# Kernel tuning notes

Hardware: AMD Instinct MI355X
Metric: run time of the kernel (lower is better)

## Reference

```python
import jax, jax.numpy as jnp
import numpy as np

C = 256
INTER = C // 2


def _conv1x1(x, w, b):
    # x: [B,C,H,W], w: [O,C], b: [O] -> [B,O,H,W]
    return jnp.einsum('bchw,oc->bohw', x, w) + b[None, :, None, None]


def setup_inputs() -> dict:
    key = jax.random.key(0)
    ks = jax.random.split(key, 9)
    B, H, W = 4, 64, 64
    x = jax.random.normal(ks[0], (B, C, H, W), dtype=jnp.float32)
    s_in = 1.0 / np.sqrt(C)
    s_int = 1.0 / np.sqrt(INTER)
    return {
        'x': x,
        'w_g': jax.random.normal(ks[1], (INTER, C), jnp.float32) * s_in,
        'b_g': jax.random.normal(ks[2], (INTER,), jnp.float32) * 0.01,
        'w_theta': jax.random.normal(ks[3], (INTER, C), jnp.float32) * s_in,
        'b_theta': jax.random.normal(ks[4], (INTER,), jnp.float32) * 0.01,
        'w_phi': jax.random.normal(ks[5], (INTER, C), jnp.float32) * s_in,
        'b_phi': jax.random.normal(ks[6], (INTER,), jnp.float32) * 0.01,
        'w_W': jax.random.normal(ks[7], (C, INTER), jnp.float32) * s_int,
        'b_W': jax.random.normal(ks[8], (C,), jnp.float32) * 0.01,
    }


def reference(x, w_g, b_g, w_theta, b_theta, w_phi, b_phi, w_W, b_W):
    B, Cc, H, W = x.shape
    N = H * W
    # 1x1 conv projections -> flatten spatial to N
    g_x = _conv1x1(x, w_g, b_g).reshape(B, INTER, N).transpose(0, 2, 1)        # [B,N,I]
    theta_x = _conv1x1(x, w_theta, b_theta).reshape(B, INTER, N).transpose(0, 2, 1)  # [B,N,I]
    phi_x = _conv1x1(x, w_phi, b_phi).reshape(B, INTER, N)                     # [B,I,N]
    f = jnp.einsum('bni,bim->bnm', theta_x, phi_x)                             # [B,N,N]
    f_div_C = jax.nn.softmax(f, axis=-1)
    y = jnp.einsum('bnm,bmi->bni', f_div_C, g_x)                               # [B,N,I]
    y = y.transpose(0, 2, 1).reshape(B, INTER, H, W)
    W_y = _conv1x1(y, w_W, b_W)                                                # [B,C,H,W]
    return W_y + x
```

## Files before the change

### kernel.cpp

```cpp
#include <hip/hip_runtime.h>

typedef unsigned short ushort_t;
typedef unsigned int uint_t;
typedef _Float16 f16;
typedef __attribute__((ext_vector_type(8))) _Float16 f16x8;
typedef __attribute__((ext_vector_type(2))) _Float16 f16x2;
typedef __attribute__((ext_vector_type(4))) float f32x4;

#define B_ 4
#define C_ 256
#define I_ 128
#define N_ 4096
#define KVB 32
#define TOT_IT (N_ / KVB)
#define LOG2E 1.44269504f

#define XT_F 0ull
#define W_F  4194304ull
#define TH_F 4325376ull
#define PH_F 6422528ull
#define G3_F 8519680ull
#define YPX_F 10616832ull

__device__ __forceinline__ float exp2_hw(float x) { return __builtin_amdgcn_exp2f(x); }
__device__ __forceinline__ float log2_hw(float x) { return __builtin_amdgcn_logf(x); }

__device__ __forceinline__ f16x2 pkrtz(float a, float b) {
    auto r = __builtin_amdgcn_cvt_pkrtz(a, b);
    f16x2 o;
    __builtin_memcpy(&o, &r, sizeof(o));
    return o;
}
__device__ __forceinline__ f32x4 mfma16h(f16x8 a, f16x8 b, f32x4 c) {
    return __builtin_amdgcn_mfma_f32_16x16x32_f16(a, b, c, 0, 0, 0);
}
__device__ __forceinline__ f32x4 zero4() { f32x4 z = {0.f, 0.f, 0.f, 0.f}; return z; }
__device__ __forceinline__ void gload_lds16(const void* g, void* lds) {
    __builtin_amdgcn_global_load_lds(
        (const __attribute__((address_space(1))) void*)g,
        (__attribute__((address_space(3))) void*)lds, 16, 0, 0);
}
__device__ __forceinline__ size_t yp_off(int s) {
    return (s < 2) ? (size_t)s * 2097152ull
                   : YPX_F + (size_t)(s - 2) * 2097152ull;
}

__global__ __launch_bounds__(256) void k_transpose_x(const float* x, const float* wg,
        const float* wt, const float* wp, const float* wW, ushort_t* ws) {
    if (blockIdx.x >= 64) {
        int idx = (((blockIdx.x - 64) * 16 + blockIdx.y * 4 + blockIdx.z) * 256
                   + threadIdx.x) * 16;
        const float* src;
        int off;
        if (idx < 32768)      { src = wg; off = idx; }
        else if (idx < 65536) { src = wt; off = idx - 32768; }
        else if (idx < 98304) { src = wp; off = idx - 65536; }
        else                  { src = wW; off = idx - 98304; }
        f16 o[16];
#pragma unroll
        for (int j = 0; j < 16; ++j) o[j] = (f16)src[off + j];
        f16* wd = (f16*)(ws + W_F);
        *(uint4*)&wd[idx]     = *(uint4*)&o[0];
        *(uint4*)&wd[idx + 8] = *(uint4*)&o[8];
        return;
    }
    __shared__ float t[64][65];
    int b = blockIdx.z, c0 = blockIdx.y * 64, n0 = blockIdx.x * 64;
    int tid = threadIdx.x;
    int cl = tid & 63, ng = tid >> 6;
    const float* xp = x + ((size_t)(b * C_ + c0 + cl)) * N_ + n0 + ng * 16;
#pragma unroll
    for (int j = 0; j < 4; ++j) {
        float4 v = ((const float4*)xp)[j];
        t[cl][ng * 16 + j * 4 + 0] = v.x;
        t[cl][ng * 16 + j * 4 + 1] = v.y;
        t[cl][ng * 16 + j * 4 + 2] = v.z;
        t[cl][ng * 16 + j * 4 + 3] = v.w;
    }
    __syncthreads();
    int cg4 = tid & 3, nr = tid >> 2;
    f16 hv[16];
#pragma unroll
    for (int k = 0; k < 16; ++k) hv[k] = (f16)t[cg4 * 16 + k][nr];
    size_t dst = ((size_t)b * N_ + n0 + nr) * C_ + c0 + cg4 * 16;
    f16* xd = (f16*)(ws + XT_F);
    *(uint4*)&xd[dst]     = *(uint4*)&hv[0];
    *(uint4*)&xd[dst + 8] = *(uint4*)&hv[8];
}

__global__ __launch_bounds__(512) void k_proj_all(const float* bg, const float* bth,
                                                  const float* bph, ushort_t* ws) {
    int b = blockIdx.y, n0 = blockIdx.x * 64;
    int w = threadIdx.x >> 6, l = threadIdx.x & 63;
    int li = l & 15, lg = l >> 4;
    int wn = (w & 3) * 16;
    int ihb = (w >> 2) * 4;
    const f16* xh = (const f16*)(ws + XT_F);
    const f16* wf = (const f16*)(ws + W_F);

    f32x4 acc[3][4];
#pragma unroll
    for (int p = 0; p < 3; ++p)
#pragma unroll
        for (int t = 0; t < 4; ++t) acc[p][t] = zero4();

    size_t arow = ((size_t)b * N_ + n0 + wn + li) * C_;
#pragma unroll 2
    for (int kb = 0; kb < 8; ++kb) {
        int kc = kb * 32 + 8 * lg;
        f16x8 ah = *(const f16x8*)&xh[arow + kc];
#pragma unroll
        for (int p = 0; p < 3; ++p)
#pragma unroll
            for (int t = 0; t < 4; ++t) {
                f16x8 bw = *(const f16x8*)&wf[(size_t)p * 32768
                               + (size_t)((ihb + t) * 16 + li) * C_ + kc];
                acc[p][t] = mfma16h(ah, bw, acc[p][t]);
            }
    }
    f16* g3p = (f16*)(ws + G3_F);
    f16* thp = (f16*)(ws + TH_F);
    f16* php = (f16*)(ws + PH_F);
#pragma unroll
    for (int p = 0; p < 3; ++p) {
        const float* bias = (p == 0) ? bg : (p == 1) ? bth : bph;
#pragma unroll
        for (int t = 0; t < 4; ++t) {
            int i = (ihb + t) * 16 + li;
            float bs = bias[i];
#pragma unroll
            for (int r = 0; r < 4; ++r) {
                int n = n0 + wn + 4 * lg + r;
                float v = acc[p][t][r] + bs;
                if (p == 0) {
                    int tq = (n >> 2) & 3;
                    size_t gi = ((size_t)b * (N_ / 32) + (n >> 5)) * 4096
                              + (size_t)(tq * 128 + (i ^ (tq << 1))) * 8
                              + ((n >> 4) & 1) * 4 + (n & 3);
                    g3p[gi] = (f16)v;
                } else if (p == 1)
                    thp[((size_t)b * N_ + n) * I_ + i] = (f16)(v * LOG2E);
                else
                    php[((size_t)b * N_ + n) * I_ + i] = (f16)v;
            }
        }
    }
}

__global__ __launch_bounds__(256, 3) void k_attn(ushort_t* ws, float* lse, int splits) {
    __shared__ __align__(16) ushort_t smem[16384];
    int b = blockIdx.y, sp = blockIdx.z;
    int w = threadIdx.x >> 6, l = threadIdx.x & 63;
    int li = l & 15, lg = l >> 4;
    int q0 = blockIdx.x * 128 + w * 16;
    const f16* th = (const f16*)(ws + TH_F);
    const f16* ph = (const f16*)(ws + PH_F);
    const f16* g3 = (const f16*)(ws + G3_F);
    f16* yp = (f16*)ws + yp_off(sp);

    f16x8 qA[4], qB[4];
#pragma unroll
    for (int kb = 0; kb < 4; ++kb) {
        qA[kb] = *(const f16x8*)&th[((size_t)b * N_ + q0 + li) * I_ + kb * 32 + 8 * lg];
        qB[kb] = *(const f16x8*)&th[((size_t)b * N_ + q0 + 64 + li) * I_ + kb * 32 + 8 * lg];
    }

    f32x4 yA[8], yB[8];
#pragma unroll
    for (int dt = 0; dt < 8; ++dt) { yA[dt] = zero4(); yB[dt] = zero4(); }
    float mA = -1e30f, lA = 0.f, mB = -1e30f, lB = 0.f;

    int beg = (sp * TOT_IT) / splits;
    int end = ((sp + 1) * TOT_IT) / splits;
    int nit = end - beg;
    int srow = l >> 4;
    size_t sp0 = ((size_t)b * N_ + w * 8 + srow) * I_ + ((l & 15) ^ srow) * 8;
    size_t sp1 = ((size_t)b * N_ + w * 8 + 4 + srow) * I_ + (((l & 15) ^ srow) ^ 4) * 8;
    size_t sg0 = (size_t)b * (N_ / 32) * 4096 + w * 1024 + l * 8;

    auto stage = [&](int kv0, int bufsel) {
        int bo = bufsel * 4096;
        gload_lds16(ph + (size_t)kv0 * I_ + sp0, smem + bo + w * 1024);
        gload_lds16(ph + (size_t)kv0 * I_ + sp1, smem + bo + w * 1024 + 512);
        gload_lds16(g3 + sg0 + (size_t)kv0 * 128, smem + 8192 + bo + w * 1024);
        gload_lds16(g3 + sg0 + (size_t)kv0 * 128 + 512,
                    smem + 8192 + bo + w * 1024 + 512);
    };

    stage(beg * KVB, 0);
    __syncthreads();

    for (int it = 0; it < nit; ++it) {
        int buf = it & 1;
        if (it + 1 < nit) stage((beg + it + 1) * KVB, buf ^ 1);
        const f16* pb = (const f16*)(smem + buf * 4096);
        const f16* gbf = (const f16*)(smem + 8192 + buf * 4096);

        f32x4 fA0 = zero4(), fA1 = zero4(), fB0 = zero4(), fB1 = zero4();
        __builtin_amdgcn_s_setprio(1);
#pragma unroll
        for (int kb = 0; kb < 4; ++kb) {
            int cc = ((kb * 4 + lg) ^ (li & 7)) * 8;
            f16x8 a0 = *(const f16x8*)&pb[li * 128 + cc];
            f16x8 a1 = *(const f16x8*)&pb[(16 + li) * 128 + cc];
            fA0 = mfma16h(a0, qA[kb], fA0);
            fB0 = mfma16h(a0, qB[kb], fB0);
            fA1 = mfma16h(a1, qA[kb], fA1);
            fB1 = mfma16h(a1, qB[kb], fB1);
        }
        __builtin_amdgcn_s_setprio(0);

        float tmA = fmaxf(fmaxf(fmaxf(fA0[0], fA0[1]), fmaxf(fA0[2], fA0[3])),
                          fmaxf(fmaxf(fA1[0], fA1[1]), fmaxf(fA1[2], fA1[3])));
        tmA = fmaxf(tmA, __shfl_xor(tmA, 16));
        tmA = fmaxf(tmA, __shfl_xor(tmA, 32));
        if (__ballot(tmA > mA + 11.0f)) {
            float mn = fmaxf(mA, tmA);
            float sc = exp2_hw(mA - mn);
            lA *= sc; mA = mn;
            float s0 = __shfl(sc, 4 * lg + 0);
            float s1 = __shfl(sc, 4 * lg + 1);
            float s2 = __shfl(sc, 4 * lg + 2);
            float s3 = __shfl(sc, 4 * lg + 3);
#pragma unroll
            for (int dt = 0; dt < 8; ++dt) {
                yA[dt][0] *= s0; yA[dt][1] *= s1; yA[dt][2] *= s2; yA[dt][3] *= s3;
            }
        }
#pragma unroll
        for (int r = 0; r < 4; ++r) {
            fA0[r] = exp2_hw(fA0[r] - mA); lA += fA0[r];
            fA1[r] = exp2_hw(fA1[r] - mA); lA += fA1[r];
        }
        union PU { f16x2 h2[4]; f16x8 v; };
        PU pA;
        pA.h2[0] = pkrtz(fA0[0], fA0[1]); pA.h2[1] = pkrtz(fA0[2], fA0[3]);
        pA.h2[2] = pkrtz(fA1[0], fA1[1]); pA.h2[3] = pkrtz(fA1[2], fA1[3]);

        float tmB = fmaxf(fmaxf(fmaxf(fB0[0], fB0[1]), fmaxf(fB0[2], fB0[3])),
                          fmaxf(fmaxf(fB1[0], fB1[1]), fmaxf(fB1[2], fB1[3])));
        tmB = fmaxf(tmB, __shfl_xor(tmB, 16));
        tmB = fmaxf(tmB, __shfl_xor(tmB, 32));
        if (__ballot(tmB > mB + 11.0f)) {
            float mn = fmaxf(mB, tmB);
            float sc = exp2_hw(mB - mn);
            lB *= sc; mB = mn;
            float s0 = __shfl(sc, 4 * lg + 0);
            float s1 = __shfl(sc, 4 * lg + 1);
            float s2 = __shfl(sc, 4 * lg + 2);
            float s3 = __shfl(sc, 4 * lg + 3);
#pragma unroll
            for (int dt = 0; dt < 8; ++dt) {
                yB[dt][0] *= s0; yB[dt][1] *= s1; yB[dt][2] *= s2; yB[dt][3] *= s3;
            }
        }
#pragma unroll
        for (int r = 0; r < 4; ++r) {
            fB0[r] = exp2_hw(fB0[r] - mB); lB += fB0[r];
            fB1[r] = exp2_hw(fB1[r] - mB); lB += fB1[r];
        }
        PU pB;
        pB.h2[0] = pkrtz(fB0[0], fB0[1]); pB.h2[1] = pkrtz(fB0[2], fB0[3]);
        pB.h2[2] = pkrtz(fB1[0], fB1[1]); pB.h2[3] = pkrtz(fB1[2], fB1[3]);

        __builtin_amdgcn_s_setprio(1);
#pragma unroll
        for (int dt = 0; dt < 8; ++dt) {
            int i = dt * 16 + li;
            f16x8 gv = *(const f16x8*)&gbf[(size_t)(lg * 128 + (i ^ (lg << 1))) * 8];
            yA[dt] = mfma16h(pA.v, gv, yA[dt]);
            yB[dt] = mfma16h(pB.v, gv, yB[dt]);
        }
        __builtin_amdgcn_s_setprio(0);
        __syncthreads();
    }

    lA += __shfl_xor(lA, 16); lA += __shfl_xor(lA, 32);
    lB += __shfl_xor(lB, 16); lB += __shfl_xor(lB, 32);
    {
        float inv = 1.0f / lA;
        float i0 = __shfl(inv, 4 * lg + 0);
        float i1 = __shfl(inv, 4 * lg + 1);
        float i2 = __shfl(inv, 4 * lg + 2);
        float i3 = __shfl(inv, 4 * lg + 3);
#pragma unroll
        for (int dt = 0; dt < 8; ++dt) {
            size_t base = ((size_t)b * N_ + q0 + 4 * lg) * I_ + dt * 16 + li;
            yp[base]          = (f16)(yA[dt][0] * i0);
            yp[base + I_]     = (f16)(yA[dt][1] * i1);
            yp[base + 2 * I_] = (f16)(yA[dt][2] * i2);
            yp[base + 3 * I_] = (f16)(yA[dt][3] * i3);
        }
    }
    {
        float inv = 1.0f / lB;
        float i0 = __shfl(inv, 4 * lg + 0);
        float i1 = __shfl(inv, 4 * lg + 1);
        float i2 = __shfl(inv, 4 * lg + 2);
        float i3 = __shfl(inv, 4 * lg + 3);
#pragma unroll
        for (int dt = 0; dt < 8; ++dt) {
            size_t base = ((size_t)b * N_ + q0 + 64 + 4 * lg) * I_ + dt * 16 + li;
            yp[base]          = (f16)(yB[dt][0] * i0);
            yp[base + I_]     = (f16)(yB[dt][1] * i1);
            yp[base + 2 * I_] = (f16)(yB[dt][2] * i2);
            yp[base + 3 * I_] = (f16)(yB[dt][3] * i3);
        }
    }
    if (l < 16) {
        lse[((size_t)sp * B_ + b) * N_ + q0 + l]      = mA + log2_hw(lA);
        lse[((size_t)sp * B_ + b) * N_ + q0 + 64 + l] = mB + log2_hw(lB);
    }
}

__global__ __launch_bounds__(512) void k_out(const float* x, const float* bW,
        const ushort_t* ws, const float* lse, float* out, int splits) {
    __shared__ __align__(16) f16 ylds[64 * 136];
    int b = blockIdx.y, n0 = blockIdx.x * 64;
    int tid = threadIdx.x;
    {
        int nn = tid >> 3, ig = tid & 7;
        size_t lrow = (size_t)b * N_ + n0 + nn;
        float mx = -1e30f;
        for (int s = 0; s < splits; ++s)
            mx = fmaxf(mx, lse[(size_t)s * (B_ * N_) + lrow]);
        float sum = 0.f;
        for (int s = 0; s < splits; ++s)
            sum += exp2_hw(lse[(size_t)s * (B_ * N_) + lrow] - mx);
        float inv = 1.0f / sum;
        float acc[16];
#pragma unroll
        for (int j = 0; j < 16; ++j) acc[j] = 0.f;
        for (int s = 0; s < splits; ++s) {
            float wg = exp2_hw(lse[(size_t)s * (B_ * N_) + lrow] - mx) * inv;
            const f16* p = (const f16*)ws + yp_off(s) + lrow * I_ + ig * 16;
            f16x8 v0 = *(const f16x8*)p;
            f16x8 v1 = *(const f16x8*)(p + 8);
#pragma unroll
            for (int j = 0; j < 8; ++j) {
                acc[j]     += wg * (float)v0[j];
                acc[8 + j] += wg * (float)v1[j];
            }
        }
        f16 o[16];
#pragma unroll
        for (int j = 0; j < 16; ++j) o[j] = (f16)acc[j];
        *(uint4*)&ylds[nn * 136 + ig * 16]     = *(uint4*)&o[0];
        *(uint4*)&ylds[nn * 136 + ig * 16 + 8] = *(uint4*)&o[8];
    }
    __syncthreads();

    int w = tid >> 6, l = tid & 63;
    int li = l & 15, lg = l >> 4;
    int cw = (w >> 1) * 64, nh = (w & 1) * 32;
    const f16* wfp = (const f16*)(ws + W_F) + 98304;

    f32x4 acc2[4][2];
#pragma unroll
    for (int mm = 0; mm < 4; ++mm)
#pragma unroll
        for (int n = 0; n < 2; ++n) acc2[mm][n] = zero4();

#pragma unroll 2
    for (int kb = 0; kb < 4; ++kb) {
        int kc = kb * 32 + 8 * lg;
        f16x8 a[4], byv[2];
#pragma unroll
        for (int mm = 0; mm < 4; ++mm)
            a[mm] = *(const f16x8*)&wfp[(size_t)(cw + mm * 16 + li) * I_ + kc];
#pragma unroll
        for (int n = 0; n < 2; ++n)
            byv[n] = *(const f16x8*)&ylds[(nh + n * 16 + li) * 136 + kc];
#pragma unroll
        for (int mm = 0; mm < 4; ++mm)
#pragma unroll
            for (int n = 0; n < 2; ++n)
                acc2[mm][n] = mfma16h(a[mm], byv[n], acc2[mm][n]);
    }
#pragma unroll
    for (int mm = 0; mm < 4; ++mm)
#pragma unroll
        for (int n = 0; n < 2; ++n)
#pragma unroll
            for (int r = 0; r < 4; ++r) {
                int c = cw + mm * 16 + lg * 4 + r;
                int nn = n0 + nh + n * 16 + li;
                size_t xi = ((size_t)b * C_ + c) * N_ + nn;
                out[xi] = acc2[mm][n][r] + bW[c] + x[xi];
            }
}

extern "C" void kernel_launch(void* const* d_in, const int* in_sizes, int n_in,
                              void* d_out, int out_size, void* d_ws, size_t ws_size,
                              hipStream_t stream) {
    const float* x  = (const float*)d_in[0];
    const float* wg = (const float*)d_in[1];
    const float* bg = (const float*)d_in[2];
    const float* wt = (const float*)d_in[3];
    const float* bt = (const float*)d_in[4];
    const float* wp = (const float*)d_in[5];
    const float* bp = (const float*)d_in[6];
    const float* wW = (const float*)d_in[7];
    const float* bW = (const float*)d_in[8];
    ushort_t* ws = (ushort_t*)d_ws;
    float* out = (float*)d_out;

    int splits = (ws_size >= 46923776ull) ? 8
               : (ws_size >= 38404096ull) ? 6 : 4;
    size_t lse_off = 2ull * (YPX_F + (size_t)(splits - 2) * 2097152ull);
    float* lse = (float*)((char*)d_ws + lse_off);

    k_transpose_x<<<dim3(66, 4, 4), 256, 0, stream>>>(x, wg, wt, wp, wW, ws);
    k_proj_all<<<dim3(64, 4), 512, 0, stream>>>(bg, bt, bp, ws);
    k_attn<<<dim3(32, 4, splits), 256, 0, stream>>>(ws, lse, splits);
    k_out<<<dim3(64, 4), 512, 0, stream>>>(x, bW, ws, lse, out, splits);
}
```

Before: 110.2 us.

## Fuse x transpose into projection, unroll attention loop, raise attn occupancy

Combines the x transpose/convert with the projection GEMM, so x is transposed through LDS inside the projection kernel and the fp16 transposed copy of x is no longer written to and read back from global memory. The attention loop is manually unrolled two-way with fixed buffer offsets and precomputed LDS offsets, which removes per-iteration index arithmetic. The attention kernel's launch bound is raised to 4 blocks per SIMD. The workspace layout is compacted and a 7-split option is added. The fused kernel adds LDS use and barriers per block, and the higher occupancy target may force register spills.

```diff
diff --git a/kernel.cpp b/kernel.cpp
--- a/kernel.cpp
+++ b/kernel.cpp
@@ -15,12 +15,11 @@
 #define TOT_IT (N_ / KVB)
 #define LOG2E 1.44269504f
 
-#define XT_F 0ull
-#define W_F  4194304ull
-#define TH_F 4325376ull
-#define PH_F 6422528ull
-#define G3_F 8519680ull
-#define YPX_F 10616832ull
+#define W_F  0ull
+#define TH_F 131072ull
+#define PH_F 2228224ull
+#define G3_F 4325376ull
+#define YP_F 6422528ull
 
 __device__ __forceinline__ float exp2_hw(float x) { return __builtin_amdgcn_exp2f(x); }
 __device__ __forceinline__ float log2_hw(float x) { return __builtin_amdgcn_logf(x); }
@@ -40,82 +39,76 @@
         (const __attribute__((address_space(1))) void*)g,
         (__attribute__((address_space(3))) void*)lds, 16, 0, 0);
 }
-__device__ __forceinline__ size_t yp_off(int s) {
-    return (s < 2) ? (size_t)s * 2097152ull
-                   : YPX_F + (size_t)(s - 2) * 2097152ull;
-}
-
-__global__ __launch_bounds__(256) void k_transpose_x(const float* x, const float* wg,
-        const float* wt, const float* wp, const float* wW, ushort_t* ws) {
-    if (blockIdx.x >= 64) {
-        int idx = (((blockIdx.x - 64) * 16 + blockIdx.y * 4 + blockIdx.z) * 256
-                   + threadIdx.x) * 16;
-        const float* src;
-        int off;
-        if (idx < 32768)      { src = wg; off = idx; }
-        else if (idx < 65536) { src = wt; off = idx - 32768; }
-        else if (idx < 98304) { src = wp; off = idx - 65536; }
-        else                  { src = wW; off = idx - 98304; }
-        f16 o[16];
-#pragma unroll
-        for (int j = 0; j < 16; ++j) o[j] = (f16)src[off + j];
-        f16* wd = (f16*)(ws + W_F);
-        *(uint4*)&wd[idx]     = *(uint4*)&o[0];
-        *(uint4*)&wd[idx + 8] = *(uint4*)&o[8];
-        return;
-    }
+
+__global__ __launch_bounds__(256) void k_convert_w(const float* wg, const float* wt,
+                                                   const float* wp, const float* wW,
+                                                   ushort_t* ws) {
+    int idx = (blockIdx.x * 256 + threadIdx.x) * 16;
+    const float* src;
+    int off;
+    if (idx < 32768)      { src = wg; off = idx; }
+    else if (idx < 65536) { src = wt; off = idx - 32768; }
+    else if (idx < 98304) { src = wp; off = idx - 65536; }
+    else                  { src = wW; off = idx - 98304; }
+    f16 o[16];
+#pragma unroll
+    for (int j = 0; j < 16; ++j) o[j] = (f16)src[off + j];
+    f16* wd = (f16*)(ws + W_F);
+    *(uint4*)&wd[idx]     = *(uint4*)&o[0];
+    *(uint4*)&wd[idx + 8] = *(uint4*)&o[8];
+}
+
+__global__ __launch_bounds__(512) void k_projx(const float* x, const float* bg,
+        const float* bth, const float* bph, ushort_t* ws) {
     __shared__ float t[64][65];
-    int b = blockIdx.z, c0 = blockIdx.y * 64, n0 = blockIdx.x * 64;
+    __shared__ __align__(16) f16 xt[64][280];
+    int b = blockIdx.y, n0 = blockIdx.x * 64;
     int tid = threadIdx.x;
-    int cl = tid & 63, ng = tid >> 6;
-    const float* xp = x + ((size_t)(b * C_ + c0 + cl)) * N_ + n0 + ng * 16;
-#pragma unroll
-    for (int j = 0; j < 4; ++j) {
-        float4 v = ((const float4*)xp)[j];
-        t[cl][ng * 16 + j * 4 + 0] = v.x;
-        t[cl][ng * 16 + j * 4 + 1] = v.y;
-        t[cl][ng * 16 + j * 4 + 2] = v.z;
-        t[cl][ng * 16 + j * 4 + 3] = v.w;
-    }
-    __syncthreads();
-    int cg4 = tid & 3, nr = tid >> 2;
-    f16 hv[16];
-#pragma unroll
-    for (int k = 0; k < 16; ++k) hv[k] = (f16)t[cg4 * 16 + k][nr];
-    size_t dst = ((size_t)b * N_ + n0 + nr) * C_ + c0 + cg4 * 16;
-    f16* xd = (f16*)(ws + XT_F);
-    *(uint4*)&xd[dst]     = *(uint4*)&hv[0];
-    *(uint4*)&xd[dst + 8] = *(uint4*)&hv[8];
-}
-
-__global__ __launch_bounds__(512) void k_proj_all(const float* bg, const float* bth,
-                                                  const float* bph, ushort_t* ws) {
-    int b = blockIdx.y, n0 = blockIdx.x * 64;
-    int w = threadIdx.x >> 6, l = threadIdx.x & 63;
+
+    for (int q = 0; q < 4; ++q) {
+        int c0 = q * 64;
+#pragma unroll
+        for (int p = 0; p < 2; ++p) {
+            int row = p * 32 + (tid >> 4);
+            int col4 = (tid & 15) * 4;
+            float4 v = *(const float4*)(x + ((size_t)(b * C_ + c0 + row)) * N_ + n0 + col4);
+            t[row][col4 + 0] = v.x; t[row][col4 + 1] = v.y;
+            t[row][col4 + 2] = v.z; t[row][col4 + 3] = v.w;
+        }
+        __syncthreads();
+        {
+            int nl = tid & 63, cg = tid >> 6;
+            f16 hv[8];
+#pragma unroll
+            for (int k = 0; k < 8; ++k) hv[k] = (f16)t[cg * 8 + k][nl];
+            *(uint4*)&xt[nl][c0 + cg * 8] = *(uint4*)&hv[0];
+        }
+        __syncthreads();
+    }
+
+    int w = tid >> 6, l = tid & 63;
     int li = l & 15, lg = l >> 4;
     int wn = (w & 3) * 16;
     int ihb = (w >> 2) * 4;
-    const f16* xh = (const f16*)(ws + XT_F);
     const f16* wf = (const f16*)(ws + W_F);
 
     f32x4 acc[3][4];
 #pragma unroll
     for (int p = 0; p < 3; ++p)
 #pragma unroll
-        for (int t = 0; t < 4; ++t) acc[p][t] = zero4();
-
-    size_t arow = ((size_t)b * N_ + n0 + wn + li) * C_;
+        for (int t2 = 0; t2 < 4; ++t2) acc[p][t2] = zero4();
+
 #pragma unroll 2
     for (int kb = 0; kb < 8; ++kb) {
         int kc = kb * 32 + 8 * lg;
-        f16x8 ah = *(const f16x8*)&xh[arow + kc];
+        f16x8 ah = *(const f16x8*)&xt[wn + li][kc];
 #pragma unroll
         for (int p = 0; p < 3; ++p)
 #pragma unroll
-            for (int t = 0; t < 4; ++t) {
+            for (int t2 = 0; t2 < 4; ++t2) {
                 f16x8 bw = *(const f16x8*)&wf[(size_t)p * 32768
-                               + (size_t)((ihb + t) * 16 + li) * C_ + kc];
-                acc[p][t] = mfma16h(ah, bw, acc[p][t]);
+                               + (size_t)((ihb + t2) * 16 + li) * C_ + kc];
+                acc[p][t2] = mfma16h(ah, bw, acc[p][t2]);
             }
     }
     f16* g3p = (f16*)(ws + G3_F);
@@ -125,13 +118,13 @@
     for (int p = 0; p < 3; ++p) {
         const float* bias = (p == 0) ? bg : (p == 1) ? bth : bph;
 #pragma unroll
-        for (int t = 0; t < 4; ++t) {
-            int i = (ihb + t) * 16 + li;
+        for (int t2 = 0; t2 < 4; ++t2) {
+            int i = (ihb + t2) * 16 + li;
             float bs = bias[i];
 #pragma unroll
             for (int r = 0; r < 4; ++r) {
                 int n = n0 + wn + 4 * lg + r;
-                float v = acc[p][t][r] + bs;
+                float v = acc[p][t2][r] + bs;
                 if (p == 0) {
                     int tq = (n >> 2) & 3;
                     size_t gi = ((size_t)b * (N_ / 32) + (n >> 5)) * 4096
@@ -147,7 +140,7 @@
     }
 }
 
-__global__ __launch_bounds__(256, 3) void k_attn(ushort_t* ws, float* lse, int splits) {
+__global__ __launch_bounds__(256, 4) void k_attn(ushort_t* ws, float* lse, int splits) {
     __shared__ __align__(16) ushort_t smem[16384];
     int b = blockIdx.y, sp = blockIdx.z;
     int w = threadIdx.x >> 6, l = threadIdx.x & 63;
@@ -156,7 +149,8 @@
     const f16* th = (const f16*)(ws + TH_F);
     const f16* ph = (const f16*)(ws + PH_F);
     const f16* g3 = (const f16*)(ws + G3_F);
-    f16* yp = (f16*)ws + yp_off(sp);
+    f16* yp = (f16*)(ws + YP_F) + (size_t)sp * 2097152ull;
+    const f16* smf = (const f16*)smem;
 
     f16x8 qA[4], qB[4];
 #pragma unroll
@@ -164,6 +158,17 @@
         qA[kb] = *(const f16x8*)&th[((size_t)b * N_ + q0 + li) * I_ + kb * 32 + 8 * lg];
         qB[kb] = *(const f16x8*)&th[((size_t)b * N_ + q0 + 64 + li) * I_ + kb * 32 + 8 * lg];
     }
+
+    int phOff[8], gOff[8];
+#pragma unroll
+    for (int kb = 0; kb < 4; ++kb) {
+        int cc = ((kb * 4 + lg) ^ (li & 7)) * 8;
+        phOff[kb * 2 + 0] = li * 128 + cc;
+        phOff[kb * 2 + 1] = (16 + li) * 128 + cc;
+    }
+#pragma unroll
+    for (int dt = 0; dt < 8; ++dt)
+        gOff[dt] = 8192 + (lg * 128 + ((dt * 16 + li) ^ (lg << 1))) * 8;
 
     f32x4 yA[8], yB[8];
 #pragma unroll
@@ -174,106 +179,116 @@
     int end = ((sp + 1) * TOT_IT) / splits;
     int nit = end - beg;
     int srow = l >> 4;
-    size_t sp0 = ((size_t)b * N_ + w * 8 + srow) * I_ + ((l & 15) ^ srow) * 8;
-    size_t sp1 = ((size_t)b * N_ + w * 8 + 4 + srow) * I_ + (((l & 15) ^ srow) ^ 4) * 8;
-    size_t sg0 = (size_t)b * (N_ / 32) * 4096 + w * 1024 + l * 8;
-
-    auto stage = [&](int kv0, int bufsel) {
-        int bo = bufsel * 4096;
-        gload_lds16(ph + (size_t)kv0 * I_ + sp0, smem + bo + w * 1024);
-        gload_lds16(ph + (size_t)kv0 * I_ + sp1, smem + bo + w * 1024 + 512);
-        gload_lds16(g3 + sg0 + (size_t)kv0 * 128, smem + 8192 + bo + w * 1024);
-        gload_lds16(g3 + sg0 + (size_t)kv0 * 128 + 512,
-                    smem + 8192 + bo + w * 1024 + 512);
-    };
-
-    stage(beg * KVB, 0);
+    const f16* srcP0 = ph + ((size_t)b * N_ + w * 8 + srow) * I_
+                          + ((l & 15) ^ srow) * 8 + (size_t)beg * KVB * I_;
+    const f16* srcP1 = ph + ((size_t)b * N_ + w * 8 + 4 + srow) * I_
+                          + (((l & 15) ^ srow) ^ 4) * 8 + (size_t)beg * KVB * I_;
+    const f16* srcG  = g3 + (size_t)b * (N_ / 32) * 4096 + w * 1024 + l * 8
+                          + (size_t)beg * KVB * 128;
+
+    gload_lds16(srcP0, smem + w * 1024);
+    gload_lds16(srcP1, smem + w * 1024 + 512);
+    gload_lds16(srcG,       smem + 8192 + w * 1024);
+    gload_lds16(srcG + 512, smem + 8192 + w * 1024 + 512);
+    srcP0 += 4096; srcP1 += 4096; srcG += 4096;
     __syncthreads();
 
-    for (int it = 0; it < nit; ++it) {
-        int buf = it & 1;
-        if (it + 1 < nit) stage((beg + it + 1) * KVB, buf ^ 1);
-        const f16* pb = (const f16*)(smem + buf * 4096);
-        const f16* gbf = (const f16*)(smem + 8192 + buf * 4096);
-
-        f32x4 fA0 = zero4(), fA1 = zero4(), fB0 = zero4(), fB1 = zero4();
-        __builtin_amdgcn_s_setprio(1);
-#pragma unroll
-        for (int kb = 0; kb < 4; ++kb) {
-            int cc = ((kb * 4 + lg) ^ (li & 7)) * 8;
-            f16x8 a0 = *(const f16x8*)&pb[li * 128 + cc];
-            f16x8 a1 = *(const f16x8*)&pb[(16 + li) * 128 + cc];
-            fA0 = mfma16h(a0, qA[kb], fA0);
-            fB0 = mfma16h(a0, qB[kb], fB0);
-            fA1 = mfma16h(a1, qA[kb], fA1);
-            fB1 = mfma16h(a1, qB[kb], fB1);
-        }
-        __builtin_amdgcn_s_setprio(0);
-
-        float tmA = fmaxf(fmaxf(fmaxf(fA0[0], fA0[1]), fmaxf(fA0[2], fA0[3])),
-                          fmaxf(fmaxf(fA1[0], fA1[1]), fmaxf(fA1[2], fA1[3])));
-        tmA = fmaxf(tmA, __shfl_xor(tmA, 16));
-        tmA = fmaxf(tmA, __shfl_xor(tmA, 32));
-        if (__ballot(tmA > mA + 11.0f)) {
-            float mn = fmaxf(mA, tmA);
-            float sc = exp2_hw(mA - mn);
-            lA *= sc; mA = mn;
-            float s0 = __shfl(sc, 4 * lg + 0);
-            float s1 = __shfl(sc, 4 * lg + 1);
-            float s2 = __shfl(sc, 4 * lg + 2);
-            float s3 = __shfl(sc, 4 * lg + 3);
-#pragma unroll
-            for (int dt = 0; dt < 8; ++dt) {
-                yA[dt][0] *= s0; yA[dt][1] *= s1; yA[dt][2] *= s2; yA[dt][3] *= s3;
-            }
-        }
-#pragma unroll
-        for (int r = 0; r < 4; ++r) {
-            fA0[r] = exp2_hw(fA0[r] - mA); lA += fA0[r];
-            fA1[r] = exp2_hw(fA1[r] - mA); lA += fA1[r];
-        }
-        union PU { f16x2 h2[4]; f16x8 v; };
-        PU pA;
-        pA.h2[0] = pkrtz(fA0[0], fA0[1]); pA.h2[1] = pkrtz(fA0[2], fA0[3]);
-        pA.h2[2] = pkrtz(fA1[0], fA1[1]); pA.h2[3] = pkrtz(fA1[2], fA1[3]);
-
-        float tmB = fmaxf(fmaxf(fmaxf(fB0[0], fB0[1]), fmaxf(fB0[2], fB0[3])),
-                          fmaxf(fmaxf(fB1[0], fB1[1]), fmaxf(fB1[2], fB1[3])));
-        tmB = fmaxf(tmB, __shfl_xor(tmB, 16));
-        tmB = fmaxf(tmB, __shfl_xor(tmB, 32));
-        if (__ballot(tmB > mB + 11.0f)) {
-            float mn = fmaxf(mB, tmB);
-            float sc = exp2_hw(mB - mn);
-            lB *= sc; mB = mn;
-            float s0 = __shfl(sc, 4 * lg + 0);
-            float s1 = __shfl(sc, 4 * lg + 1);
-            float s2 = __shfl(sc, 4 * lg + 2);
-            float s3 = __shfl(sc, 4 * lg + 3);
-#pragma unroll
-            for (int dt = 0; dt < 8; ++dt) {
-                yB[dt][0] *= s0; yB[dt][1] *= s1; yB[dt][2] *= s2; yB[dt][3] *= s3;
-            }
-        }
-#pragma unroll
-        for (int r = 0; r < 4; ++r) {
-            fB0[r] = exp2_hw(fB0[r] - mB); lB += fB0[r];
-            fB1[r] = exp2_hw(fB1[r] - mB); lB += fB1[r];
-        }
-        PU pB;
-        pB.h2[0] = pkrtz(fB0[0], fB0[1]); pB.h2[1] = pkrtz(fB0[2], fB0[3]);
-        pB.h2[2] = pkrtz(fB1[0], fB1[1]); pB.h2[3] = pkrtz(fB1[2], fB1[3]);
-
-        __builtin_amdgcn_s_setprio(1);
-#pragma unroll
-        for (int dt = 0; dt < 8; ++dt) {
-            int i = dt * 16 + li;
-            f16x8 gv = *(const f16x8*)&gbf[(size_t)(lg * 128 + (i ^ (lg << 1))) * 8];
-            yA[dt] = mfma16h(pA.v, gv, yA[dt]);
-            yB[dt] = mfma16h(pB.v, gv, yB[dt]);
-        }
-        __builtin_amdgcn_s_setprio(0);
-        __syncthreads();
-    }
+#define ATTN_STEP(BUF, HASNEXT)                                                   \
+    do {                                                                          \
+        if (HASNEXT) {                                                            \
+            gload_lds16(srcP0, smem + ((BUF) ^ 4096) + w * 1024);                 \
+            gload_lds16(srcP1, smem + ((BUF) ^ 4096) + w * 1024 + 512);           \
+            gload_lds16(srcG,       smem + 8192 + ((BUF) ^ 4096) + w * 1024);     \
+            gload_lds16(srcG + 512, smem + 8192 + ((BUF) ^ 4096) + w * 1024 + 512);\
+            srcP0 += 4096; srcP1 += 4096; srcG += 4096;                           \
+        }                                                                         \
+        f32x4 fA0 = zero4(), fA1 = zero4(), fB0 = zero4(), fB1 = zero4();         \
+        __builtin_amdgcn_s_setprio(1);                                            \
+        _Pragma("unroll")                                                         \
+        for (int kb = 0; kb < 4; ++kb) {                                          \
+            f16x8 a0 = *(const f16x8*)&smf[phOff[kb * 2 + 0] + (BUF)];            \
+            f16x8 a1 = *(const f16x8*)&smf[phOff[kb * 2 + 1] + (BUF)];            \
+            fA0 = mfma16h(a0, qA[kb], fA0);                                       \
+            fB0 = mfma16h(a0, qB[kb], fB0);                                       \
+            fA1 = mfma16h(a1, qA[kb], fA1);                                       \
+            fB1 = mfma16h(a1, qB[kb], fB1);                                       \
+        }                                                                         \
+        __builtin_amdgcn_s_setprio(0);                                            \
+        float tmA = fmaxf(fmaxf(fmaxf(fA0[0], fA0[1]), fmaxf(fA0[2], fA0[3])),    \
+                          fmaxf(fmaxf(fA1[0], fA1[1]), fmaxf(fA1[2], fA1[3])));   \
+        tmA = fmaxf(tmA, __shfl_xor(tmA, 16));                                    \
+        tmA = fmaxf(tmA, __shfl_xor(tmA, 32));                                    \
+        if (__ballot(tmA > mA + 11.0f)) {                                         \
+            float mn = fmaxf(mA, tmA);                                            \
+            float sc = exp2_hw(mA - mn);                                          \
+            lA *= sc; mA = mn;                                                    \
+            float s0 = __shfl(sc, 4 * lg + 0);                                    \
+            float s1 = __shfl(sc, 4 * lg + 1);                                    \
+            float s2 = __shfl(sc, 4 * lg + 2);                                    \
+            float s3 = __shfl(sc, 4 * lg + 3);                                    \
+            _Pragma("unroll")                                                     \
+            for (int dt = 0; dt < 8; ++dt) {                                      \
+                yA[dt][0] *= s0; yA[dt][1] *= s1;                                 \
+                yA[dt][2] *= s2; yA[dt][3] *= s3;                                 \
+            }                                                                     \
+        }                                                                         \
+        _Pragma("unroll")                                                         \
+        for (int r = 0; r < 4; ++r) {                                             \
+            fA0[r] = exp2_hw(fA0[r] - mA);                                        \
+            fA1[r] = exp2_hw(fA1[r] - mA);                                        \
+        }                                                                         \
+        lA += ((fA0[0] + fA0[1]) + (fA0[2] + fA0[3]))                             \
+            + ((fA1[0] + fA1[1]) + (fA1[2] + fA1[3]));                            \
+        union PU { f16x2 h2[4]; f16x8 v; };                                       \
+        PU pA, pB;                                                                \
+        pA.h2[0] = pkrtz(fA0[0], fA0[1]); pA.h2[1] = pkrtz(fA0[2], fA0[3]);       \
+        pA.h2[2] = pkrtz(fA1[0], fA1[1]); pA.h2[3] = pkrtz(fA1[2], fA1[3]);       \
+        float tmB = fmaxf(fmaxf(fmaxf(fB0[0], fB0[1]), fmaxf(fB0[2], fB0[3])),    \
+                          fmaxf(fmaxf(fB1[0], fB1[1]), fmaxf(fB1[2], fB1[3])));   \
+        tmB = fmaxf(tmB, __shfl_xor(tmB, 16));                                    \
+        tmB = fmaxf(tmB, __shfl_xor(tmB, 32));                                    \
+        if (__ballot(tmB > mB + 11.0f)) {                                         \
+            float mn = fmaxf(mB, tmB);                                            \
+            float sc = exp2_hw(mB - mn);                                          \
+            lB *= sc; mB = mn;                                                    \
+            float s0 = __shfl(sc, 4 * lg + 0);                                    \
+            float s1 = __shfl(sc, 4 * lg + 1);                                    \
+            float s2 = __shfl(sc, 4 * lg + 2);                                    \
+            float s3 = __shfl(sc, 4 * lg + 3);                                    \
+            _Pragma("unroll")                                                     \
+            for (int dt = 0; dt < 8; ++dt) {                                      \
+                yB[dt][0] *= s0; yB[dt][1] *= s1;                                 \
+                yB[dt][2] *= s2; yB[dt][3] *= s3;                                 \
+            }                                                                     \
+        }                                                                         \
+        _Pragma("unroll")                                                         \
+        for (int r = 0; r < 4; ++r) {                                             \
+            fB0[r] = exp2_hw(fB0[r] - mB);                                        \
+            fB1[r] = exp2_hw(fB1[r] - mB);                                        \
+        }                                                                         \
+        lB += ((fB0[0] + fB0[1]) + (fB0[2] + fB0[3]))                             \
+            + ((fB1[0] + fB1[1]) + (fB1[2] + fB1[3]));                            \
+        pB.h2[0] = pkrtz(fB0[0], fB0[1]); pB.h2[1] = pkrtz(fB0[2], fB0[3]);       \
+        pB.h2[2] = pkrtz(fB1[0], fB1[1]); pB.h2[3] = pkrtz(fB1[2], fB1[3]);       \
+        __builtin_amdgcn_s_setprio(1);                                            \
+        _Pragma("unroll")                                                         \
+        for (int dt = 0; dt < 8; ++dt) {                                          \
+            f16x8 gv = *(const f16x8*)&smf[gOff[dt] + (BUF)];                     \
+            yA[dt] = mfma16h(pA.v, gv, yA[dt]);                                   \
+            yB[dt] = mfma16h(pB.v, gv, yB[dt]);                                   \
+        }                                                                         \
+        __builtin_amdgcn_s_setprio(0);                                            \
+        __syncthreads();                                                          \
+    } while (0)
+
+    int it = 0;
+    while (it + 2 <= nit) {
+        ATTN_STEP(0, (it + 1 < nit));
+        ATTN_STEP(4096, (it + 2 < nit));
+        it += 2;
+    }
+    if (it < nit) ATTN_STEP(0, false);
+#undef ATTN_STEP
 
     lA += __shfl_xor(lA, 16); lA += __shfl_xor(lA, 32);
     lB += __shfl_xor(lB, 16); lB += __shfl_xor(lB, 32);
@@ -333,7 +348,8 @@
         for (int j = 0; j < 16; ++j) acc[j] = 0.f;
         for (int s = 0; s < splits; ++s) {
             float wg = exp2_hw(lse[(size_t)s * (B_ * N_) + lrow] - mx) * inv;
-            const f16* p = (const f16*)ws + yp_off(s) + lrow * I_ + ig * 16;
+            const f16* p = (const f16*)(ws + YP_F) + (size_t)s * 2097152ull
+                         + lrow * I_ + ig * 16;
             f16x8 v0 = *(const f16x8*)p;
             f16x8 v1 = *(const f16x8*)(p + 8);
 #pragma unroll
@@ -406,12 +422,13 @@
     float* out = (float*)d_out;
 
     int splits = (ws_size >= 46923776ull) ? 8
+               : (ws_size >= 42663936ull) ? 7
                : (ws_size >= 38404096ull) ? 6 : 4;
-    size_t lse_off = 2ull * (YPX_F + (size_t)(splits - 2) * 2097152ull);
+    size_t lse_off = 2ull * (YP_F + (size_t)splits * 2097152ull);
     float* lse = (float*)((char*)d_ws + lse_off);
 
-    k_transpose_x<<<dim3(66, 4, 4), 256, 0, stream>>>(x, wg, wt, wp, wW, ws);
-    k_proj_all<<<dim3(64, 4), 512, 0, stream>>>(bg, bt, bp, ws);
+    k_convert_w<<<32, 256, 0, stream>>>(wg, wt, wp, wW, ws);
+    k_projx<<<dim3(64, 4), 512, 0, stream>>>(x, bg, bt, bp, ws);
     k_attn<<<dim3(32, 4, splits), 256, 0, stream>>>(ws, lse, splits);
     k_out<<<dim3(64, 4), 512, 0, stream>>>(x, bW, ws, lse, out, splits);
 }
```

Result: slower. 173.1 us (+57.0%).
